# Optimization experiments

Measured on AMD Instinct MI355X. Metric: run time of the kernel, lower is better.

Reference implementation:

```python
import jax, jax.numpy as jnp
import numpy as np

D, BEV_H, BEV_W, NH, NP = 256, 200, 200, 8, 8
NQ = BEV_H * BEV_W
DFF = 1024
HD = D // NH


def setup_inputs() -> dict:
    key = jax.random.key(0)
    ks = jax.random.split(key, 12)
    def rn(k, shape, scale=0.02):
        return jax.random.normal(k, shape, jnp.float32) * scale
    return dict(
        B_adj0=rn(ks[0], (1, NQ, D), 1.0),
        B_adj1=rn(ks[1], (1, NQ, D), 1.0),
        query_embed=rn(ks[2], (NQ, D), 1.0),
        W_ref=rn(ks[3], (D, 2)), b_ref=jnp.zeros((2,), jnp.float32),
        W_off=rn(ks[4], (D, NH * NP * 2)), b_off=rn(ks[5], (NH * NP * 2,), 0.5),
        W_attn=rn(ks[6], (D, NH * NP)), b_attn=jnp.zeros((NH * NP,), jnp.float32),
        W_val=rn(ks[7], (D, D)), b_val=jnp.zeros((D,), jnp.float32),
        W_out=rn(ks[8], (D, D)), b_out=jnp.zeros((D,), jnp.float32),
        W_ffn1=rn(ks[9], (D, DFF)), b_ffn1=jnp.zeros((DFF,), jnp.float32),
        W_ffn2=rn(ks[10], (DFF, D)), b_ffn2=jnp.zeros((D,), jnp.float32),
    )


def _deform_attend(value, loc, attn_w):
    """Bilinear-sample `value` (bs,NQ,NH,HD laid out as BEV_H x BEV_W map) at
    normalized locations loc (bs,nq,NH,NP,2) with align_corners=False and zero
    padding (torch grid_sample semantics), weighted by attn_w (bs,nq,NH,NP)."""
    bs, _, nh, hd = value.shape
    nq = loc.shape[1]
    vt = value.transpose(0, 2, 1, 3)  # (bs, nh, HW, hd)
    # grid = 2*loc - 1 ; pixel = ((grid+1)*size - 1)/2 = loc*size - 0.5
    x = loc[..., 0] * BEV_W - 0.5
    y = loc[..., 1] * BEV_H - 0.5
    x0f = jnp.floor(x); y0f = jnp.floor(y)
    lx = x - x0f; ly = y - y0f
    x0 = x0f.astype(jnp.int32); y0 = y0f.astype(jnp.int32)
    acc = jnp.zeros((bs, nh, nq, hd), value.dtype)
    corners = ((0, 0, (1 - lx) * (1 - ly)), (1, 0, lx * (1 - ly)),
               (0, 1, (1 - lx) * ly), (1, 1, lx * ly))
    for dx, dy, w in corners:
        ix = x0 + dx
        iy = y0 + dy
        valid = ((ix >= 0) & (ix < BEV_W) & (iy >= 0) & (iy < BEV_H)).astype(value.dtype)
        idx = jnp.clip(iy, 0, BEV_H - 1) * BEV_W + jnp.clip(ix, 0, BEV_W - 1)  # (bs,nq,nh,np)
        idx_t = idx.transpose(0, 2, 1, 3).reshape(bs, nh, nq * NP)
        v = jnp.take_along_axis(vt, idx_t[..., None], axis=2).reshape(bs, nh, nq, NP, hd)
        wt = (w * valid * attn_w).transpose(0, 2, 1, 3)  # (bs,nh,nq,np)
        acc = acc + (wt[..., None] * v).sum(3)
    return acc.transpose(0, 2, 1, 3).reshape(bs, nq, nh * hd)


def reference(B_adj0, B_adj1, query_embed, W_ref, b_ref, W_off, b_off,
              W_attn, b_attn, W_val, b_val, W_out, b_out,
              W_ffn1, b_ffn1, W_ffn2, b_ffn2):
    bs = B_adj0.shape[0]
    q = jnp.broadcast_to(query_embed[None], (bs, NQ, D))
    # reference points in [0,1]
    ref = jax.nn.sigmoid(q @ W_ref + b_ref)  # (bs,nq,2)
    off = (q @ W_off + b_off).reshape(bs, NQ, NH, NP, 2)
    attn = jax.nn.softmax((q @ W_attn + b_attn).reshape(bs, NQ, NH, NP), axis=-1)
    offset_normalizer = jnp.array([BEV_W, BEV_H], jnp.float32)
    loc = ref[:, :, None, None, :] + off / offset_normalizer  # (bs,nq,nh,np,2)
    B_short = jnp.zeros((bs, NQ, D), B_adj0.dtype)
    for V in (B_adj0, B_adj1):
        val = (V @ W_val + b_val).reshape(bs, NQ, NH, HD)
        out = _deform_attend(val, loc, attn) @ W_out + b_out
        B_short = B_short + out + q  # mmcv MSDA residual: identity = query
    # FFN with residual (mmcv FFN, add_identity=True, drop=0)
    ffn = jax.nn.relu(B_short @ W_ffn1 + b_ffn1) @ W_ffn2 + b_ffn2
    return B_short + ffn
```

## Files before the change

kernel.cpp:

```cpp
#include <hip/hip_runtime.h>
#include <hip/hip_bf16.h>

#define NQ    40000
#define DD    256
#define NHH   8
#define NPP   8
#define DFF   1024
#define BEV   200
#define MPAD  40064

typedef __attribute__((ext_vector_type(4))) float f32x4;
typedef __attribute__((ext_vector_type(8))) short s16x8;
typedef __hip_bfloat16 bf16;

#define AS1(p) ((const __attribute__((address_space(1))) void*)(p))
#define AS3(p) ((__attribute__((address_space(3))) void*)(p))

__device__ inline unsigned short f2bf(float f) {
  union { bf16 h; unsigned short u; } cv;
  cv.h = __float2bfloat16(f);
  return cv.u;
}
__device__ inline float bf2f(bf16 h) { return __bfloat162float(h); }
__device__ inline float bfs(short u) {
  union { float f; unsigned u; } c;
  c.u = ((unsigned)(unsigned short)u) << 16;
  return c.f;
}

__global__ void transpose_cvt(const float* __restrict__ src, bf16* __restrict__ dst,
                              int R, int C) {
  int i = blockIdx.x * 256 + threadIdx.x;
  if (i >= R * C) return;
  int c = i / R, r = i % R;
  dst[i] = __float2bfloat16(src[(size_t)r * C + c]);
}

__global__ void build_wq(const float* __restrict__ Woff, const float* __restrict__ Wattn,
                         const float* __restrict__ Wref, bf16* __restrict__ dst) {
  int i = blockIdx.x * 256 + threadIdx.x;
  int n = i >> 8, k = i & 255;
  float v;
  if (n < 128)      v = Woff[k * 128 + n];
  else if (n < 192) v = Wattn[k * 64 + (n - 128)];
  else if (n < 194) v = Wref[k * 2 + (n - 192)];
  else              v = 0.f;
  dst[i] = __float2bfloat16(v);
}

__global__ void cvt_bf16_kernel(const float* __restrict__ src, bf16* __restrict__ dst, int n4) {
  int i = blockIdx.x * 256 + threadIdx.x;
  if (i >= n4) return;
  float4 v = ((const float4*)src)[i];
  ushort4 o;
  o.x = f2bf(v.x); o.y = f2bf(v.y); o.z = f2bf(v.z); o.w = f2bf(v.w);
  ((ushort4*)dst)[i] = o;
}

__global__ void addcvt_kernel(const float* __restrict__ a, const float* __restrict__ b,
                              bf16* __restrict__ dst, int n4) {
  int i = blockIdx.x * 256 + threadIdx.x;
  if (i >= n4) return;
  float4 va = ((const float4*)a)[i];
  float4 vb = ((const float4*)b)[i];
  ushort4 o;
  o.x = f2bf(va.x + vb.x); o.y = f2bf(va.y + vb.y);
  o.z = f2bf(va.z + vb.z); o.w = f2bf(va.w + vb.w);
  ((ushort4*)dst)[i] = o;
}

template<int BK_, bool RELU>
__global__ void gemm_bt(const bf16* __restrict__ A, const bf16* __restrict__ Bt,
                        int K, int Ntiles, int N,
                        const float* __restrict__ bias, float biasScale,
                        const bf16* __restrict__ addB, float addScale,
                        bf16* __restrict__ outB, float* __restrict__ outF, int Mvalid) {
  constexpr int HALF = BK_ * 256;
  constexpr int ROWB = BK_ * 2;
  constexpr int BUFB = BK_ * 512;
  __shared__ __align__(16) char smem[2 * BUFB];
  const int tid  = threadIdx.x;
  const int wave = tid >> 6, lane = tid & 63;
  const int nwg = gridDim.x;
  const int orig = blockIdx.x;
  const int q8 = nwg >> 3, r8 = nwg & 7;
  const int xcd = orig & 7, idx = orig >> 3;
  const int wg = (xcd < r8 ? xcd * (q8 + 1) : r8 * (q8 + 1) + (xcd - r8) * q8) + idx;
  const int tm = wg / Ntiles, tn = wg % Ntiles;
  const int wr = wave >> 1, wc = wave & 1;

  f32x4 acc[4][4];
#pragma unroll
  for (int i = 0; i < 4; ++i)
#pragma unroll
    for (int j = 0; j < 4; ++j) {
      f32x4 z = {0.f, 0.f, 0.f, 0.f};
      acc[i][j] = z;
    }

  const char* Ab = (const char*)A;
  const char* Bb = (const char*)Bt;
  const int nK = K / BK_;

  auto stage = [&](int bufBase, int kt) {
    constexpr int WI = BK_ / 8;
#pragma unroll
    for (int i = 0; i < WI; ++i) {
      const int j  = wave * WI + i;
      const int p0 = j << 10;
      const char* g;
      if (p0 < HALF) {
        const int pl = p0 + lane * 16;
        const int row = pl / ROWB, cb = pl % ROWB;
        g = Ab + ((size_t)(tm * 128 + row) * K + kt * BK_) * 2 + cb;
      } else {
        const int pl = p0 - HALF + lane * 16;
        const int row = pl / ROWB, cb = pl % ROWB;
        g = Bb + ((size_t)(tn * 128 + row) * K + kt * BK_) * 2 + cb;
      }
      __builtin_amdgcn_global_load_lds(AS1(g), AS3(smem + bufBase + p0), 16, 0, 0);
    }
  };

  stage(0, 0);
  __syncthreads();
  int cur = 0;
  for (int kt = 0; kt < nK; ++kt) {
    if (kt + 1 < nK) stage((cur ^ 1) * BUFB, kt + 1);
    const char* sbuf = smem + cur * BUFB;
    constexpr int NKK = BK_ / 32;
#pragma unroll
    for (int kk = 0; kk < NKK; ++kk) {
      const int r  = lane & 15;
      const int kb = kk * 64 + (lane >> 4) * 16;
      s16x8 af[4], bfr[4];
#pragma unroll
      for (int mr = 0; mr < 4; ++mr)
        af[mr] = *(const s16x8*)(sbuf + (wr * 64 + mr * 16 + r) * ROWB + kb);
#pragma unroll
      for (int nr = 0; nr < 4; ++nr)
        bfr[nr] = *(const s16x8*)(sbuf + HALF + (wc * 64 + nr * 16 + r) * ROWB + kb);
#pragma unroll
      for (int mr = 0; mr < 4; ++mr)
#pragma unroll
        for (int nr = 0; nr < 4; ++nr)
          acc[mr][nr] = __builtin_amdgcn_mfma_f32_16x16x32_bf16(af[mr], bfr[nr], acc[mr][nr], 0, 0, 0);
    }
    __syncthreads();
    cur ^= 1;
  }

  const int r = lane & 15, rg = lane >> 4;
#pragma unroll
  for (int mr = 0; mr < 4; ++mr) {
#pragma unroll
    for (int nr = 0; nr < 4; ++nr) {
      const int gn = tn * 128 + wc * 64 + nr * 16 + r;
      const float bval = bias ? biasScale * bias[gn] : 0.f;
#pragma unroll
      for (int j2 = 0; j2 < 4; ++j2) {
        const int gm = tm * 128 + wr * 64 + mr * 16 + rg * 4 + j2;
        float v = acc[mr][nr][j2] + bval;
        if (addB && gm < Mvalid) v += addScale * bf2f(addB[(size_t)gm * N + gn]);
        if (RELU) v = fmaxf(v, 0.f);
        if (outB) outB[(size_t)gm * N + gn] = __float2bfloat16(v);
        if (outF && gm < Mvalid) outF[(size_t)gm * N + gn] = v;
      }
    }
  }
}

__global__ void finalize_kernel(const bf16* __restrict__ raw, const float* __restrict__ b_off,
                                const float* __restrict__ b_attn, const float* __restrict__ b_ref,
                                float* __restrict__ samp) {
  __shared__ float r[4][256];
  const int tid = threadIdx.x;
  const int q0 = blockIdx.x * 4;
#pragma unroll
  for (int i = 0; i < 4; ++i) {
    int e = tid + i * 256;
    int ql = e >> 8, k = e & 255;
    r[ql][k] = bf2f(raw[(size_t)(q0 + ql) * 256 + k]);
  }
  __syncthreads();
  const int ql = tid >> 6, hp = tid & 63;
  const int h = hp >> 3, p = hp & 7;
  float v[8];
  float m = -1e30f;
#pragma unroll
  for (int pp = 0; pp < 8; ++pp) {
    v[pp] = r[ql][128 + h * 8 + pp] + b_attn[h * 8 + pp];
    m = fmaxf(m, v[pp]);
  }
  float s = 0.f;
#pragma unroll
  for (int pp = 0; pp < 8; ++pp) { v[pp] = expf(v[pp] - m); s += v[pp]; }
  const float w = v[p] / s;
  const float sx = 1.f / (1.f + expf(-(r[ql][192] + b_ref[0])));
  const float sy = 1.f / (1.f + expf(-(r[ql][193] + b_ref[1])));
  const float px = sx * (float)BEV + (r[ql][hp * 2 + 0] + b_off[hp * 2 + 0]) - 0.5f;
  const float py = sy * (float)BEV + (r[ql][hp * 2 + 1] + b_off[hp * 2 + 1]) - 0.5f;
  const size_t o = ((size_t)(q0 + ql) * 64 + hp) * 3;
  samp[o] = px; samp[o + 1] = py; samp[o + 2] = w;
}

__global__ __launch_bounds__(256, 4)
void deform_kernel(const float* __restrict__ samp, const bf16* __restrict__ val,
                   bf16* __restrict__ out) {
  __shared__ float s[8 * 192];
  const int tid = threadIdx.x;
  const int q0 = blockIdx.x * 8;
#pragma unroll
  for (int i = 0; i < 6; ++i) {
    const int e = tid + i * 256;
    s[e] = samp[(size_t)q0 * 192 + e];
  }
  __syncthreads();
  const int ql = tid >> 5;
  const int lane5 = tid & 31;
  const int h = lane5 >> 2;
  const int dg = lane5 & 3;
  const float* sp = s + ql * 192 + h * 24;
  const bf16* vb = val + h * 32 + dg * 8;

  float acc[8] = {0.f, 0.f, 0.f, 0.f, 0.f, 0.f, 0.f, 0.f};
#pragma unroll 2
  for (int p = 0; p < 8; ++p) {
    const float px = sp[p * 3 + 0], py = sp[p * 3 + 1], w = sp[p * 3 + 2];
    const float xf = floorf(px), yf = floorf(py);
    const int x0 = (int)xf, y0 = (int)yf;
    const float lx = px - xf, ly = py - yf;
    const float xa = (x0 >= 0 && x0 < BEV) ? 1.f : 0.f;
    const float xb = (x0 + 1 >= 0 && x0 + 1 < BEV) ? 1.f : 0.f;
    const float ya = (y0 >= 0 && y0 < BEV) ? 1.f : 0.f;
    const float yb = (y0 + 1 >= 0 && y0 + 1 < BEV) ? 1.f : 0.f;
    const float w00 = w * (1.f - lx) * (1.f - ly) * xa * ya;
    const float w10 = w * lx * (1.f - ly) * xb * ya;
    const float w01 = w * (1.f - lx) * ly * xa * yb;
    const float w11 = w * lx * ly * xb * yb;
    const int cx0 = min(max(x0, 0), BEV - 1);
    const int cx1 = min(max(x0 + 1, 0), BEV - 1);
    const int cy0 = min(max(y0, 0), BEV - 1) * BEV;
    const int cy1 = min(max(y0 + 1, 0), BEV - 1) * BEV;
    const s16x8 v00 = *(const s16x8*)(vb + (size_t)(cy0 + cx0) * 256);
    const s16x8 v10 = *(const s16x8*)(vb + (size_t)(cy0 + cx1) * 256);
    const s16x8 v01 = *(const s16x8*)(vb + (size_t)(cy1 + cx0) * 256);
    const s16x8 v11 = *(const s16x8*)(vb + (size_t)(cy1 + cx1) * 256);
#pragma unroll
    for (int j = 0; j < 8; ++j) {
      acc[j] += w00 * bfs(v00[j]) + w10 * bfs(v10[j])
              + w01 * bfs(v01[j]) + w11 * bfs(v11[j]);
    }
  }
  s16x8 o;
#pragma unroll
  for (int j = 0; j < 8; ++j) o[j] = (short)f2bf(acc[j]);
  *(s16x8*)(out + (size_t)(q0 + ql) * 256 + h * 32 + dg * 8) = o;
}

extern "C" void kernel_launch(void* const* d_in, const int* in_sizes, int n_in,
                              void* d_out, int out_size, void* d_ws, size_t ws_size,
                              hipStream_t stream) {
  const float* B0     = (const float*)d_in[0];
  const float* B1     = (const float*)d_in[1];
  const float* qe     = (const float*)d_in[2];
  const float* W_ref  = (const float*)d_in[3];
  const float* b_ref  = (const float*)d_in[4];
  const float* W_off  = (const float*)d_in[5];
  const float* b_off  = (const float*)d_in[6];
  const float* W_attn = (const float*)d_in[7];
  const float* b_attn = (const float*)d_in[8];
  const float* W_val  = (const float*)d_in[9];
  const float* b_val  = (const float*)d_in[10];
  const float* W_out  = (const float*)d_in[11];
  const float* b_out  = (const float*)d_in[12];
  const float* W_ffn1 = (const float*)d_in[13];
  const float* b_ffn1 = (const float*)d_in[14];
  const float* W_ffn2 = (const float*)d_in[15];
  const float* b_ffn2 = (const float*)d_in[16];
  float* out = (float*)d_out;
  char* ws = (char*)d_ws;

  const size_t SZ_MAT = (size_t)MPAD * 256 * 2;
  const size_t VAL_OFF    = 0;
  const size_t RAW_OFF    = SZ_MAT;
  const size_t BSH_OFF    = 2 * SZ_MAT;
  const size_t H_OFF      = 3 * SZ_MAT;
  const size_t QE_OFF     = H_OFF;
  const size_t VSUM_OFF   = H_OFF + SZ_MAT;
  const size_t H_BYTES    = (size_t)MPAD * 1024 * 2;
  const size_t SAMP_OFF   = H_OFF + H_BYTES;
  const size_t SAMP_BYTES = (size_t)NQ * 192 * 4;
  const size_t WQ_OFF     = SAMP_OFF + SAMP_BYTES;
  const size_t WVAL_OFF   = WQ_OFF   + 256 * 256 * 2;
  const size_t WOUT_OFF   = WVAL_OFF + 256 * 256 * 2;
  const size_t WF1_OFF    = WOUT_OFF + 256 * 256 * 2;
  const size_t WF2_OFF    = WF1_OFF  + 1024 * 256 * 2;

  bf16* valb  = (bf16*)(ws + VAL_OFF);
  bf16* rawb  = (bf16*)(ws + RAW_OFF);
  bf16* defb  = rawb;
  bf16* bshb  = (bf16*)(ws + BSH_OFF);
  bf16* hbuf  = (bf16*)(ws + H_OFF);
  bf16* qeb   = (bf16*)(ws + QE_OFF);
  bf16* vsum  = (bf16*)(ws + VSUM_OFF);
  float* samp = (float*)(ws + SAMP_OFF);
  bf16* wq    = (bf16*)(ws + WQ_OFF);
  bf16* wval  = (bf16*)(ws + WVAL_OFF);
  bf16* wout  = (bf16*)(ws + WOUT_OFF);
  bf16* wf1   = (bf16*)(ws + WF1_OFF);
  bf16* wf2   = (bf16*)(ws + WF2_OFF);

  const int n4 = NQ * 256 / 4;
  const int MT = MPAD / 128;

  build_wq<<<256, 256, 0, stream>>>(W_off, W_attn, W_ref, wq);
  transpose_cvt<<<(256 * 256 + 255) / 256, 256, 0, stream>>>(W_val, wval, 256, 256);
  transpose_cvt<<<(256 * 256 + 255) / 256, 256, 0, stream>>>(W_out, wout, 256, 256);
  transpose_cvt<<<(256 * 1024 + 255) / 256, 256, 0, stream>>>(W_ffn1, wf1, 256, 1024);
  transpose_cvt<<<(1024 * 256 + 255) / 256, 256, 0, stream>>>(W_ffn2, wf2, 1024, 256);

  cvt_bf16_kernel<<<n4 / 256, 256, 0, stream>>>(qe, qeb, n4);
  addcvt_kernel<<<n4 / 256, 256, 0, stream>>>(B0, B1, vsum, n4);

  gemm_bt<32, false><<<MT * 2, 256, 0, stream>>>(qeb, wq, 256, 2, 256,
                                                 nullptr, 0.f, nullptr, 0.f,
                                                 rawb, nullptr, NQ);
  finalize_kernel<<<NQ / 4, 256, 0, stream>>>(rawb, b_off, b_attn, b_ref, samp);

  gemm_bt<32, false><<<MT * 2, 256, 0, stream>>>(vsum, wval, 256, 2, 256,
                                                 b_val, 2.f, nullptr, 0.f,
                                                 valb, nullptr, NQ);

  deform_kernel<<<NQ / 8, 256, 0, stream>>>(samp, valb, defb);

  gemm_bt<32, false><<<MT * 2, 256, 0, stream>>>(defb, wout, 256, 2, 256,
                                                 b_out, 2.f, qeb, 2.f,
                                                 bshb, nullptr, NQ);

  gemm_bt<32, true><<<MT * 8, 256, 0, stream>>>(bshb, wf1, 256, 8, 1024,
                                                b_ffn1, 1.f, nullptr, 0.f,
                                                hbuf, nullptr, NQ);

  gemm_bt<32, false><<<MT * 2, 256, 0, stream>>>(hbuf, wf2, 1024, 2, 256,
                                                 b_ffn2, 1.f, bshb, 1.f,
                                                 nullptr, out, NQ);
}
```

Before: 265.2 us.

## Add panel-resident A GEMM with B streamed from global for K=256 GEMMs

```diff
diff --git a/kernel.cpp b/kernel.cpp
--- a/kernel.cpp
+++ b/kernel.cpp
@@ -67,6 +67,95 @@
   o.x = f2bf(va.x + vb.x); o.y = f2bf(va.y + vb.y);
   o.z = f2bf(va.z + vb.z); o.w = f2bf(va.w + vb.w);
   ((ushort4*)dst)[i] = o;
+}
+
+template<int WPB, bool RELU>
+__global__ __launch_bounds__(WPB * 64)
+void gemm_pa(const bf16* __restrict__ A, const bf16* __restrict__ Bt,
+             int K, int Ntiles, int N,
+             const float* __restrict__ bias, float biasScale,
+             const bf16* __restrict__ addB, float addScale,
+             bf16* __restrict__ outB, float* __restrict__ outF, int Mvalid) {
+  __shared__ __align__(16) char smem[32768];
+  const int tid  = threadIdx.x;
+  const int wave = tid >> 6, lane = tid & 63;
+  const int r = lane & 15, hi = lane >> 4;
+  const int nwg = gridDim.x;
+  const int orig = blockIdx.x;
+  const int q8 = nwg >> 3, r8 = nwg & 7;
+  const int xcd = orig & 7, idx = orig >> 3;
+  const int wg = (xcd < r8 ? xcd * (q8 + 1) : r8 * (q8 + 1) + (xcd - r8) * q8) + idx;
+  const int tm = wg / Ntiles, tn = wg % Ntiles;
+  const int col0 = (tn * WPB + wave) * 64;
+
+  constexpr int SI = 32 / WPB;
+#pragma unroll
+  for (int i = 0; i < SI; ++i) {
+    const int p0 = (wave * SI + i) << 10;
+    const int pl = p0 + lane * 16;
+    const int row = pl >> 9;
+    const int chunk = (pl & 511) >> 4;
+    const char* g = (const char*)A + ((size_t)(tm * 64 + row) * K) * 2
+                  + ((chunk ^ (row & 7)) << 4);
+    __builtin_amdgcn_global_load_lds(AS1(g), AS3(smem + p0), 16, 0, 0);
+  }
+  __syncthreads();
+
+  f32x4 acc[4][4];
+#pragma unroll
+  for (int i = 0; i < 4; ++i)
+#pragma unroll
+    for (int j = 0; j < 4; ++j) {
+      f32x4 z = {0.f, 0.f, 0.f, 0.f};
+      acc[i][j] = z;
+    }
+
+  const char* Bb = (const char*)Bt;
+  s16x8 bf[4], bfn[4];
+#pragma unroll
+  for (int nf = 0; nf < 4; ++nf)
+    bf[nf] = *(const s16x8*)(Bb + ((size_t)(col0 + nf * 16 + r) * K) * 2 + hi * 16);
+#pragma unroll
+  for (int kc = 0; kc < 8; ++kc) {
+    if (kc < 7) {
+#pragma unroll
+      for (int nf = 0; nf < 4; ++nf)
+        bfn[nf] = *(const s16x8*)(Bb + ((size_t)(col0 + nf * 16 + r) * K) * 2
+                                  + (kc + 1) * 64 + hi * 16);
+    }
+    s16x8 af[4];
+#pragma unroll
+    for (int mf = 0; mf < 4; ++mf)
+      af[mf] = *(const s16x8*)(smem + (mf * 16 + r) * 512
+                               + (((kc * 4 + hi) ^ (r & 7)) << 4));
+#pragma unroll
+    for (int mf = 0; mf < 4; ++mf)
+#pragma unroll
+      for (int nf = 0; nf < 4; ++nf)
+        acc[mf][nf] = __builtin_amdgcn_mfma_f32_16x16x32_bf16(af[mf], bf[nf], acc[mf][nf], 0, 0, 0);
+    if (kc < 7) {
+#pragma unroll
+      for (int nf = 0; nf < 4; ++nf) bf[nf] = bfn[nf];
+    }
+  }
+
+#pragma unroll
+  for (int mf = 0; mf < 4; ++mf) {
+#pragma unroll
+    for (int nf = 0; nf < 4; ++nf) {
+      const int gn = col0 + nf * 16 + r;
+      const float bval = bias ? biasScale * bias[gn] : 0.f;
+#pragma unroll
+      for (int j2 = 0; j2 < 4; ++j2) {
+        const int gm = tm * 64 + mf * 16 + hi * 4 + j2;
+        float v = acc[mf][nf][j2] + bval;
+        if (addB && gm < Mvalid) v += addScale * bf2f(addB[(size_t)gm * N + gn]);
+        if (RELU) v = fmaxf(v, 0.f);
+        if (outB) outB[(size_t)gm * N + gn] = __float2bfloat16(v);
+        if (outF && gm < Mvalid) outF[(size_t)gm * N + gn] = v;
+      }
+    }
+  }
 }
 
 template<int BK_, bool RELU>
@@ -312,7 +401,8 @@
   bf16* wf2   = (bf16*)(ws + WF2_OFF);
 
   const int n4 = NQ * 256 / 4;
-  const int MT = MPAD / 128;
+  const int MT64 = MPAD / 64;
+  const int MT128 = MPAD / 128;
 
   build_wq<<<256, 256, 0, stream>>>(W_off, W_attn, W_ref, wq);
   transpose_cvt<<<(256 * 256 + 255) / 256, 256, 0, stream>>>(W_val, wval, 256, 256);
@@ -323,26 +413,26 @@
   cvt_bf16_kernel<<<n4 / 256, 256, 0, stream>>>(qe, qeb, n4);
   addcvt_kernel<<<n4 / 256, 256, 0, stream>>>(B0, B1, vsum, n4);
 
-  gemm_bt<32, false><<<MT * 2, 256, 0, stream>>>(qeb, wq, 256, 2, 256,
-                                                 nullptr, 0.f, nullptr, 0.f,
-                                                 rawb, nullptr, NQ);
+  gemm_pa<4, false><<<MT64, 256, 0, stream>>>(qeb, wq, 256, 1, 256,
+                                              nullptr, 0.f, nullptr, 0.f,
+                                              rawb, nullptr, NQ);
   finalize_kernel<<<NQ / 4, 256, 0, stream>>>(rawb, b_off, b_attn, b_ref, samp);
 
-  gemm_bt<32, false><<<MT * 2, 256, 0, stream>>>(vsum, wval, 256, 2, 256,
-                                                 b_val, 2.f, nullptr, 0.f,
-                                                 valb, nullptr, NQ);
+  gemm_pa<4, false><<<MT64, 256, 0, stream>>>(vsum, wval, 256, 1, 256,
+                                              b_val, 2.f, nullptr, 0.f,
+                                              valb, nullptr, NQ);
 
   deform_kernel<<<NQ / 8, 256, 0, stream>>>(samp, valb, defb);
 
-  gemm_bt<32, false><<<MT * 2, 256, 0, stream>>>(defb, wout, 256, 2, 256,
-                                                 b_out, 2.f, qeb, 2.f,
-                                                 bshb, nullptr, NQ);
-
-  gemm_bt<32, true><<<MT * 8, 256, 0, stream>>>(bshb, wf1, 256, 8, 1024,
-                                                b_ffn1, 1.f, nullptr, 0.f,
-                                                hbuf, nullptr, NQ);
-
-  gemm_bt<32, false><<<MT * 2, 256, 0, stream>>>(hbuf, wf2, 1024, 2, 256,
-                                                 b_ffn2, 1.f, bshb, 1.f,
-                                                 nullptr, out, NQ);
-}
+  gemm_pa<4, false><<<MT64, 256, 0, stream>>>(defb, wout, 256, 1, 256,
+                                              b_out, 2.f, qeb, 2.f,
+                                              bshb, nullptr, NQ);
+
+  gemm_pa<8, true><<<MT64 * 2, 512, 0, stream>>>(bshb, wf1, 256, 2, 1024,
+                                                 b_ffn1, 1.f, nullptr, 0.f,
+                                                 hbuf, nullptr, NQ);
+
+  gemm_bt<32, false><<<MT128 * 2, 256, 0, stream>>>(hbuf, wf2, 1024, 2, 256,
+                                                    b_ffn2, 1.f, bshb, 1.f,
+                                                    nullptr, out, NQ);
+}
```

New measurement: 301.0 us. +13.5%, slower.

## Fuse FFN GEMMs into one kernel keeping hidden activations in LDS

Applied to the files above, without the earlier changes.

```diff
diff --git a/kernel.cpp b/kernel.cpp
--- a/kernel.cpp
+++ b/kernel.cpp
@@ -48,25 +48,21 @@
   dst[i] = __float2bfloat16(v);
 }
 
-__global__ void cvt_bf16_kernel(const float* __restrict__ src, bf16* __restrict__ dst, int n4) {
+__global__ void cvt_both_kernel(const float* __restrict__ qe,
+                                const float* __restrict__ a, const float* __restrict__ b,
+                                bf16* __restrict__ qeb, bf16* __restrict__ vsum, int n4) {
   int i = blockIdx.x * 256 + threadIdx.x;
   if (i >= n4) return;
-  float4 v = ((const float4*)src)[i];
-  ushort4 o;
-  o.x = f2bf(v.x); o.y = f2bf(v.y); o.z = f2bf(v.z); o.w = f2bf(v.w);
-  ((ushort4*)dst)[i] = o;
-}
-
-__global__ void addcvt_kernel(const float* __restrict__ a, const float* __restrict__ b,
-                              bf16* __restrict__ dst, int n4) {
-  int i = blockIdx.x * 256 + threadIdx.x;
-  if (i >= n4) return;
+  float4 q4 = ((const float4*)qe)[i];
+  ushort4 oq;
+  oq.x = f2bf(q4.x); oq.y = f2bf(q4.y); oq.z = f2bf(q4.z); oq.w = f2bf(q4.w);
+  ((ushort4*)qeb)[i] = oq;
   float4 va = ((const float4*)a)[i];
   float4 vb = ((const float4*)b)[i];
   ushort4 o;
   o.x = f2bf(va.x + vb.x); o.y = f2bf(va.y + vb.y);
   o.z = f2bf(va.z + vb.z); o.w = f2bf(va.w + vb.w);
-  ((ushort4*)dst)[i] = o;
+  ((ushort4*)vsum)[i] = o;
 }
 
 template<int BK_, bool RELU>
@@ -165,6 +161,152 @@
         if (RELU) v = fmaxf(v, 0.f);
         if (outB) outB[(size_t)gm * N + gn] = __float2bfloat16(v);
         if (outF && gm < Mvalid) outF[(size_t)gm * N + gn] = v;
+      }
+    }
+  }
+}
+
+__global__ __launch_bounds__(256)
+void fused_ffn(const bf16* __restrict__ Bsh, const bf16* __restrict__ Wf1t,
+               const bf16* __restrict__ Wf2t,
+               const float* __restrict__ b1, const float* __restrict__ b2,
+               float* __restrict__ outF, int Mvalid) {
+  constexpr int BUFB = 20480;
+  __shared__ __align__(16) char smem[2 * BUFB];
+  __shared__ __align__(16) char hbuf[64 * 544];
+  const int tid  = threadIdx.x;
+  const int wave = tid >> 6, lane = tid & 63;
+  const int r = lane & 15, hi = lane >> 4;
+  const int nwg = gridDim.x;
+  const int orig = blockIdx.x;
+  const int q8 = nwg >> 3, r8_ = nwg & 7;
+  const int xcd = orig & 7, idx = orig >> 3;
+  const int tm = (xcd < r8_ ? xcd * (q8 + 1) : r8_ * (q8 + 1) + (xcd - r8_) * q8) + idx;
+
+  f32x4 acc[4][4];
+#pragma unroll
+  for (int i = 0; i < 4; ++i)
+#pragma unroll
+    for (int j = 0; j < 4; ++j) {
+      f32x4 z = {0.f, 0.f, 0.f, 0.f};
+      acc[i][j] = z;
+    }
+
+  const char* Ab = (const char*)Bsh;
+  const char* W1 = (const char*)Wf1t;
+  const char* W2 = (const char*)Wf2t;
+
+  auto stage1 = [&](int bufBase, int chunk, int kt) {
+#pragma unroll
+    for (int i = 0; i < 5; ++i) {
+      const int p0 = (wave * 5 + i) << 10;
+      const char* g;
+      if (p0 < 4096) {
+        const int pl = p0 + lane * 16;
+        const int row = pl >> 6, cb = pl & 63;
+        g = Ab + ((size_t)(tm * 64 + row) * 256 + kt * 32) * 2 + cb;
+      } else {
+        const int pl = p0 - 4096 + lane * 16;
+        const int row = pl >> 6, cb = pl & 63;
+        g = W1 + ((size_t)(chunk * 256 + row) * 256 + kt * 32) * 2 + cb;
+      }
+      __builtin_amdgcn_global_load_lds(AS1(g), AS3(smem + bufBase + p0), 16, 0, 0);
+    }
+  };
+  auto stage2 = [&](int bufBase, int chunk, int kt) {
+#pragma unroll
+    for (int i = 0; i < 4; ++i) {
+      const int p0 = (wave * 4 + i) << 10;
+      const int pl = p0 + lane * 16;
+      const int row = pl >> 6, cb = pl & 63;
+      const char* g = W2 + ((size_t)row * 1024 + chunk * 256 + kt * 32) * 2 + cb;
+      __builtin_amdgcn_global_load_lds(AS1(g), AS3(smem + bufBase + p0), 16, 0, 0);
+    }
+  };
+
+  for (int chunk = 0; chunk < 4; ++chunk) {
+    f32x4 acc_h[4][4];
+#pragma unroll
+    for (int i = 0; i < 4; ++i)
+#pragma unroll
+      for (int j = 0; j < 4; ++j) {
+        f32x4 z = {0.f, 0.f, 0.f, 0.f};
+        acc_h[i][j] = z;
+      }
+    stage1(0, chunk, 0);
+    __syncthreads();
+    int cur = 0;
+    for (int kt = 0; kt < 8; ++kt) {
+      if (kt + 1 < 8) stage1((cur ^ 1) * BUFB, chunk, kt + 1);
+      const char* sbuf = smem + cur * BUFB;
+      const int kb = hi * 16;
+      s16x8 af[4], bfr[4];
+#pragma unroll
+      for (int mr = 0; mr < 4; ++mr)
+        af[mr] = *(const s16x8*)(sbuf + (mr * 16 + r) * 64 + kb);
+#pragma unroll
+      for (int nr = 0; nr < 4; ++nr)
+        bfr[nr] = *(const s16x8*)(sbuf + 4096 + (wave * 64 + nr * 16 + r) * 64 + kb);
+#pragma unroll
+      for (int mr = 0; mr < 4; ++mr)
+#pragma unroll
+        for (int nr = 0; nr < 4; ++nr)
+          acc_h[mr][nr] = __builtin_amdgcn_mfma_f32_16x16x32_bf16(af[mr], bfr[nr], acc_h[mr][nr], 0, 0, 0);
+      __syncthreads();
+      cur ^= 1;
+    }
+#pragma unroll
+    for (int nr = 0; nr < 4; ++nr) {
+      const int hcol = wave * 64 + nr * 16 + r;
+      const float bv = b1[chunk * 256 + hcol];
+#pragma unroll
+      for (int mr = 0; mr < 4; ++mr)
+#pragma unroll
+        for (int j2 = 0; j2 < 4; ++j2) {
+          const int row = mr * 16 + hi * 4 + j2;
+          const float v = fmaxf(acc_h[mr][nr][j2] + bv, 0.f);
+          *(unsigned short*)(hbuf + row * 544 + hcol * 2) = f2bf(v);
+        }
+    }
+    __syncthreads();
+    stage2(0, chunk, 0);
+    __syncthreads();
+    cur = 0;
+    for (int kt = 0; kt < 8; ++kt) {
+      if (kt + 1 < 8) stage2((cur ^ 1) * BUFB, chunk, kt + 1);
+      const char* sbuf = smem + cur * BUFB;
+      const int kb = hi * 16;
+      s16x8 af[4], bfr[4];
+#pragma unroll
+      for (int mr = 0; mr < 4; ++mr)
+        af[mr] = *(const s16x8*)(hbuf + (mr * 16 + r) * 544 + kt * 64 + kb);
+#pragma unroll
+      for (int nr = 0; nr < 4; ++nr)
+        bfr[nr] = *(const s16x8*)(sbuf + (wave * 64 + nr * 16 + r) * 64 + kb);
+#pragma unroll
+      for (int mr = 0; mr < 4; ++mr)
+#pragma unroll
+        for (int nr = 0; nr < 4; ++nr)
+          acc[mr][nr] = __builtin_amdgcn_mfma_f32_16x16x32_bf16(af[mr], bfr[nr], acc[mr][nr], 0, 0, 0);
+      __syncthreads();
+      cur ^= 1;
+    }
+    __syncthreads();
+  }
+
+#pragma unroll
+  for (int mr = 0; mr < 4; ++mr) {
+#pragma unroll
+    for (int nr = 0; nr < 4; ++nr) {
+      const int gn = wave * 64 + nr * 16 + r;
+      const float bval = b2[gn];
+#pragma unroll
+      for (int j2 = 0; j2 < 4; ++j2) {
+        const int gm = tm * 64 + mr * 16 + hi * 4 + j2;
+        if (gm < Mvalid) {
+          float v = acc[mr][nr][j2] + bval + bf2f(Bsh[(size_t)gm * 256 + gn]);
+          outF[(size_t)gm * 256 + gn] = v;
+        }
       }
     }
   }
@@ -285,11 +427,9 @@
   const size_t VAL_OFF    = 0;
   const size_t RAW_OFF    = SZ_MAT;
   const size_t BSH_OFF    = 2 * SZ_MAT;
-  const size_t H_OFF      = 3 * SZ_MAT;
-  const size_t QE_OFF     = H_OFF;
-  const size_t VSUM_OFF   = H_OFF + SZ_MAT;
-  const size_t H_BYTES    = (size_t)MPAD * 1024 * 2;
-  const size_t SAMP_OFF   = H_OFF + H_BYTES;
+  const size_t QE_OFF     = 3 * SZ_MAT;
+  const size_t VSUM_OFF   = 4 * SZ_MAT;
+  const size_t SAMP_OFF   = 5 * SZ_MAT;
   const size_t SAMP_BYTES = (size_t)NQ * 192 * 4;
   const size_t WQ_OFF     = SAMP_OFF + SAMP_BYTES;
   const size_t WVAL_OFF   = WQ_OFF   + 256 * 256 * 2;
@@ -301,7 +441,6 @@
   bf16* rawb  = (bf16*)(ws + RAW_OFF);
   bf16* defb  = rawb;
   bf16* bshb  = (bf16*)(ws + BSH_OFF);
-  bf16* hbuf  = (bf16*)(ws + H_OFF);
   bf16* qeb   = (bf16*)(ws + QE_OFF);
   bf16* vsum  = (bf16*)(ws + VSUM_OFF);
   float* samp = (float*)(ws + SAMP_OFF);
@@ -312,7 +451,8 @@
   bf16* wf2   = (bf16*)(ws + WF2_OFF);
 
   const int n4 = NQ * 256 / 4;
-  const int MT = MPAD / 128;
+  const int MT64 = MPAD / 64;
+  const int MT128 = MPAD / 128;
 
   build_wq<<<256, 256, 0, stream>>>(W_off, W_attn, W_ref, wq);
   transpose_cvt<<<(256 * 256 + 255) / 256, 256, 0, stream>>>(W_val, wval, 256, 256);
@@ -320,29 +460,22 @@
   transpose_cvt<<<(256 * 1024 + 255) / 256, 256, 0, stream>>>(W_ffn1, wf1, 256, 1024);
   transpose_cvt<<<(1024 * 256 + 255) / 256, 256, 0, stream>>>(W_ffn2, wf2, 1024, 256);
 
-  cvt_bf16_kernel<<<n4 / 256, 256, 0, stream>>>(qe, qeb, n4);
-  addcvt_kernel<<<n4 / 256, 256, 0, stream>>>(B0, B1, vsum, n4);
-
-  gemm_bt<32, false><<<MT * 2, 256, 0, stream>>>(qeb, wq, 256, 2, 256,
-                                                 nullptr, 0.f, nullptr, 0.f,
-                                                 rawb, nullptr, NQ);
+  cvt_both_kernel<<<n4 / 256, 256, 0, stream>>>(qe, B0, B1, qeb, vsum, n4);
+
+  gemm_bt<32, false><<<MT128 * 2, 256, 0, stream>>>(qeb, wq, 256, 2, 256,
+                                                    nullptr, 0.f, nullptr, 0.f,
+                                                    rawb, nullptr, NQ);
   finalize_kernel<<<NQ / 4, 256, 0, stream>>>(rawb, b_off, b_attn, b_ref, samp);
 
-  gemm_bt<32, false><<<MT * 2, 256, 0, stream>>>(vsum, wval, 256, 2, 256,
-                                                 b_val, 2.f, nullptr, 0.f,
-                                                 valb, nullptr, NQ);
+  gemm_bt<32, false><<<MT128 * 2, 256, 0, stream>>>(vsum, wval, 256, 2, 256,
+                                                    b_val, 2.f, nullptr, 0.f,
+                                                    valb, nullptr, NQ);
 
   deform_kernel<<<NQ / 8, 256, 0, stream>>>(samp, valb, defb);
 
-  gemm_bt<32, false><<<MT * 2, 256, 0, stream>>>(defb, wout, 256, 2, 256,
-                                                 b_out, 2.f, qeb, 2.f,
-                                                 bshb, nullptr, NQ);
-
-  gemm_bt<32, true><<<MT * 8, 256, 0, stream>>>(bshb, wf1, 256, 8, 1024,
-                                                b_ffn1, 1.f, nullptr, 0.f,
-                                                hbuf, nullptr, NQ);
-
-  gemm_bt<32, false><<<MT * 2, 256, 0, stream>>>(hbuf, wf2, 1024, 2, 256,
-                                                 b_ffn2, 1.f, bshb, 1.f,
-                                                 nullptr, out, NQ);
-}
+  gemm_bt<32, false><<<MT128 * 2, 256, 0, stream>>>(defb, wout, 256, 2, 256,
+                                                    b_out, 2.f, qeb, 2.f,
+                                                    bshb, nullptr, NQ);
+
+  fused_ffn<<<MT64, 256, 0, stream>>>(bshb, wf1, wf2, b_ffn1, b_ffn2, out, NQ);
+}
```

New measurement: 269.1 us. No clear change (+1.5%).
